# Optimization experiments

Hardware: AMD Instinct MI355X
Metric: run time of the kernel (lower is better)

## Reference

```python
import jax, jax.numpy as jnp
import numpy as np

N = 100000
E = 3200000
NFEAT, NHID, NCLASS = 512, 64, 64
K = 10
ALPHA = 0.1


def setup_inputs() -> dict:
    key = jax.random.key(0)
    ks = jax.random.split(key, 8)
    x = jax.random.normal(ks[0], (N, NFEAT), dtype=jnp.float32)
    edge_index = jax.random.randint(ks[1], (2, E), 0, N, dtype=jnp.int32)
    s1 = 1.0 / np.sqrt(NFEAT)
    W1 = jax.random.uniform(ks[2], (NFEAT, NHID), jnp.float32, -s1, s1)
    b1 = jax.random.uniform(ks[3], (NHID,), jnp.float32, -s1, s1)
    s2 = 1.0 / np.sqrt(NHID)
    W2 = jax.random.uniform(ks[4], (NHID, NCLASS), jnp.float32, -s2, s2)
    b2 = jax.random.uniform(ks[5], (NCLASS,), jnp.float32, -s2, s2)
    # PPR init of gamma coefficients: temp[k] = alpha*(1-alpha)^k, temp[K] = (1-alpha)^K
    temp = ALPHA * (1.0 - ALPHA) ** np.arange(K + 1)
    temp[-1] = (1.0 - ALPHA) ** K
    temp = jnp.asarray(temp, dtype=jnp.float32)
    return {"x": x, "edge_index": edge_index, "W1": W1, "b1": b1, "W2": W2, "b2": b2, "temp": temp}


def _gcn_norm(edge_index, num_nodes):
    # add self loops, weight 1 (PyG gcn_norm defaults)
    loop = jnp.arange(num_nodes, dtype=edge_index.dtype)
    src = jnp.concatenate([edge_index[0], loop])
    dst = jnp.concatenate([edge_index[1], loop])
    w = jnp.ones(src.shape[0], dtype=jnp.float32)
    deg = jax.ops.segment_sum(w, dst, num_segments=num_nodes)
    dinv = jnp.where(deg > 0, jax.lax.rsqrt(deg), 0.0)
    norm = dinv[src] * w * dinv[dst]
    return src, dst, norm


def reference(x, edge_index, W1, b1, W2, b2, temp):
    # MLP part (eval mode, dropout is identity)
    h = jax.nn.relu(x @ W1 + b1) @ W2 + b2  # [N, nclass]
    src, dst, norm = _gcn_norm(edge_index, x.shape[0])
    hidden = h * temp[0]
    for k in range(K):
        # gather-scale-scatter: h <- A_hat @ h
        h = jax.ops.segment_sum(norm[:, None] * h[src], dst, num_segments=x.shape[0])
        hidden = hidden + temp[k + 1] * h
    return hidden
```

## Files before the change

### kernel.cpp

```cpp
#include <hip/hip_runtime.h>

static constexpr int N = 100000;
static constexpr int E = 3200000;
static constexpr int NFEAT = 512;
static constexpr int K = 10;

typedef _Float16 half8 __attribute__((ext_vector_type(8)));
typedef _Float16 half4v __attribute__((ext_vector_type(4)));

static constexpr size_t OFF_CNT    = 0;
static constexpr size_t OFF_FILL   = 512ull * 1024;
static constexpr size_t OFF_ROWPTR = 1024ull * 1024;
static constexpr size_t OFF_DINV   = 1536ull * 1024;
static constexpr size_t OFF_BSUM   = 2048ull * 1024;
static constexpr size_t OFF_EW     = 2560ull * 1024;
static constexpr size_t OFF_GA     = OFF_EW + (size_t)E * 4 + 1024;
static constexpr size_t OFF_GB     = OFF_GA + (size_t)N * 64 * 2 + 1024;
static constexpr size_t OFF_H1     = OFF_GB + (size_t)N * 64 * 2 + 1024;

__global__ __launch_bounds__(256) void count_k(const int* __restrict__ dst,
                                               int* __restrict__ cnt) {
  int e = blockIdx.x * 256 + threadIdx.x;
  if (e < E) atomicAdd(&cnt[__builtin_nontemporal_load(dst + e)], 1);
}

__global__ __launch_bounds__(256) void dinv_k(const int* __restrict__ cnt,
                                              float* __restrict__ dinv) {
  int i = blockIdx.x * 256 + threadIdx.x;
  if (i < N) dinv[i] = 1.0f / sqrtf((float)(cnt[i] + 1));
}

__device__ inline int wave_incl_scan(int x) {
  int lane = threadIdx.x & 63;
#pragma unroll
  for (int off = 1; off < 64; off <<= 1) {
    int y = __shfl_up(x, off, 64);
    if (lane >= off) x += y;
  }
  return x;
}

__global__ __launch_bounds__(256) void scan1_k(const int* __restrict__ cnt,
                                               int* __restrict__ rowptr,
                                               int* __restrict__ bsum) {
  __shared__ int wsum[4];
  int tid = threadIdx.x, wid = tid >> 6, lane = tid & 63;
  int base = blockIdx.x * 1024 + tid * 4;
  int4 v = {0, 0, 0, 0};
  if (base + 3 < N) {
    v = *(const int4*)(cnt + base);
  } else {
    if (base + 0 < N) v.x = cnt[base + 0];
    if (base + 1 < N) v.y = cnt[base + 1];
    if (base + 2 < N) v.z = cnt[base + 2];
    if (base + 3 < N) v.w = cnt[base + 3];
  }
  int tsum = v.x + v.y + v.z + v.w;
  int incl = wave_incl_scan(tsum);
  if (lane == 63) wsum[wid] = incl;
  __syncthreads();
  int wof = 0;
  for (int i = 0; i < wid; ++i) wof += wsum[i];
  int e0 = wof + incl - tsum;
  if (base + 0 < N) rowptr[base + 0] = e0;
  if (base + 1 < N) rowptr[base + 1] = e0 + v.x;
  if (base + 2 < N) rowptr[base + 2] = e0 + v.x + v.y;
  if (base + 3 < N) rowptr[base + 3] = e0 + v.x + v.y + v.z;
  if (tid == 255) bsum[blockIdx.x] = wof + incl;
}

__global__ __launch_bounds__(128) void scan2_k(int* __restrict__ bsum) {
  __shared__ int w0sum;
  int tid = threadIdx.x, wid = tid >> 6, lane = tid & 63;
  int v = (tid < 98) ? bsum[tid] : 0;
  int incl = wave_incl_scan(v);
  if (wid == 0 && lane == 63) w0sum = incl;
  __syncthreads();
  int excl = incl - v + (wid ? w0sum : 0);
  if (tid < 98) bsum[tid] = excl;
}

__global__ __launch_bounds__(256) void scan3_k(int* __restrict__ rowptr,
                                               const int* __restrict__ bsum) {
  int i = blockIdx.x * 256 + threadIdx.x;
  if (i < N) rowptr[i] += bsum[blockIdx.x >> 2];
  if (i == 0) rowptr[N] = E;
}

__global__ __launch_bounds__(256) void fill2_k(const int* __restrict__ src,
                                               const int* __restrict__ dst,
                                               const int* __restrict__ rowptr,
                                               int* __restrict__ fillc,
                                               int* __restrict__ ew) {
  const int slice = blockIdx.x & 7;
  const int chunk = blockIdx.x >> 3;
  const int lo = slice * 12500;
  const int hi = lo + 12500;
  int e = chunk * 4096 + threadIdx.x;
  const int eend = min(E, chunk * 4096 + 4096);
  for (; e < eend; e += 256) {
    int d = __builtin_nontemporal_load(dst + e);
    if (d >= lo && d < hi) {
      int pos = rowptr[d] + atomicAdd(&fillc[d], 1);
      ew[pos] = __builtin_nontemporal_load(src + e);
    }
  }
}

__global__ __launch_bounds__(256) void gemm1_k(const float* __restrict__ x,
                                               const float* __restrict__ W1,
                                               const float* __restrict__ b1,
                                               float* __restrict__ h1) {
  __shared__ float xs[16][256];
  __shared__ float w1s[16 * 64];
  const int tid = threadIdx.x;
  const int n0 = blockIdx.x * 256;
  const int tn = tid & 127;
  const int jh = tid >> 7;
  float4 acca[8], accb[8];
#pragma unroll
  for (int i = 0; i < 8; ++i) {
    acca[i] = float4{0.f, 0.f, 0.f, 0.f};
    accb[i] = float4{0.f, 0.f, 0.f, 0.f};
  }
  const int rowA = min(n0 + tid, N - 1);
  const float* xr = x + (size_t)rowA * NFEAT;
  for (int k0 = 0; k0 < NFEAT; k0 += 16) {
    float4 a0 = *(const float4*)(xr + k0 + 0);
    float4 a1 = *(const float4*)(xr + k0 + 4);
    float4 a2 = *(const float4*)(xr + k0 + 8);
    float4 a3 = *(const float4*)(xr + k0 + 12);
    float4 wv = *(const float4*)(W1 + (size_t)k0 * 64 + tid * 4);
    __syncthreads();
    xs[0][tid] = a0.x;  xs[1][tid] = a0.y;  xs[2][tid] = a0.z;  xs[3][tid] = a0.w;
    xs[4][tid] = a1.x;  xs[5][tid] = a1.y;  xs[6][tid] = a1.z;  xs[7][tid] = a1.w;
    xs[8][tid] = a2.x;  xs[9][tid] = a2.y;  xs[10][tid] = a2.z; xs[11][tid] = a2.w;
    xs[12][tid] = a3.x; xs[13][tid] = a3.y; xs[14][tid] = a3.z; xs[15][tid] = a3.w;
    *(float4*)&w1s[tid * 4] = wv;
    __syncthreads();
#pragma unroll
    for (int kk = 0; kk < 16; ++kk) {
      float xa = xs[kk][tn];
      float xb = xs[kk][tn + 128];
      const float* wr = &w1s[kk * 64 + jh * 32];
#pragma unroll
      for (int jj = 0; jj < 8; ++jj) {
        float4 w4 = *(const float4*)(wr + jj * 4);
        acca[jj].x += xa * w4.x; acca[jj].y += xa * w4.y;
        acca[jj].z += xa * w4.z; acca[jj].w += xa * w4.w;
        accb[jj].x += xb * w4.x; accb[jj].y += xb * w4.y;
        accb[jj].z += xb * w4.z; accb[jj].w += xb * w4.w;
      }
    }
  }
  const int na = n0 + tn, nb = na + 128;
#pragma unroll
  for (int jj = 0; jj < 8; ++jj) {
    int j = jh * 32 + jj * 4;
    float4 bb = *(const float4*)(b1 + j);
    float4 ra, rb;
    ra.x = fmaxf(acca[jj].x + bb.x, 0.f); ra.y = fmaxf(acca[jj].y + bb.y, 0.f);
    ra.z = fmaxf(acca[jj].z + bb.z, 0.f); ra.w = fmaxf(acca[jj].w + bb.w, 0.f);
    rb.x = fmaxf(accb[jj].x + bb.x, 0.f); rb.y = fmaxf(accb[jj].y + bb.y, 0.f);
    rb.z = fmaxf(accb[jj].z + bb.z, 0.f); rb.w = fmaxf(accb[jj].w + bb.w, 0.f);
    if (na < N) *(float4*)(h1 + (size_t)na * 64 + j) = ra;
    if (nb < N) *(float4*)(h1 + (size_t)nb * 64 + j) = rb;
  }
}

__global__ __launch_bounds__(256) void gemm2_k(const float* __restrict__ h1,
                                               const float* __restrict__ W2,
                                               const float* __restrict__ b2,
                                               const float* __restrict__ temp,
                                               const float* __restrict__ dinv,
                                               _Float16* __restrict__ g0,
                                               float* __restrict__ out) {
  __shared__ float w2s[64 * 64];
  const int tid = threadIdx.x;
#pragma unroll
  for (int i = 0; i < 4; ++i)
    *(float4*)&w2s[(i * 256 + tid) * 4] = *(const float4*)(W2 + (size_t)(i * 256 + tid) * 4);
  __syncthreads();
  const int node = blockIdx.x * 256 + tid;
  if (node >= N) return;
  float4 acc[16];
#pragma unroll
  for (int c = 0; c < 16; ++c) acc[c] = *(const float4*)(b2 + c * 4);
  const float* hr = h1 + (size_t)node * 64;
  for (int j0 = 0; j0 < 64; j0 += 4) {
    float4 hv = *(const float4*)(hr + j0);
    float hv4[4] = {hv.x, hv.y, hv.z, hv.w};
#pragma unroll
    for (int l = 0; l < 4; ++l) {
      const float* wr = &w2s[(j0 + l) * 64];
#pragma unroll
      for (int c = 0; c < 16; ++c) {
        float4 w4 = *(const float4*)(wr + c * 4);
        acc[c].x += hv4[l] * w4.x; acc[c].y += hv4[l] * w4.y;
        acc[c].z += hv4[l] * w4.z; acc[c].w += hv4[l] * w4.w;
      }
    }
  }
  const float t0 = temp[0];
  const float di = dinv[node];
  _Float16* gp = g0 + (size_t)node * 64;
  float* op = out + (size_t)node * 64;
#pragma unroll
  for (int c = 0; c < 16; ++c) {
    float4 o;
    o.x = t0 * acc[c].x; o.y = t0 * acc[c].y;
    o.z = t0 * acc[c].z; o.w = t0 * acc[c].w;
    *(float4*)(op + c * 4) = o;
    half4v g;
    g[0] = (_Float16)(di * acc[c].x); g[1] = (_Float16)(di * acc[c].y);
    g[2] = (_Float16)(di * acc[c].z); g[3] = (_Float16)(di * acc[c].w);
    *(half4v*)(gp + c * 4) = g;
  }
}

__global__ __launch_bounds__(256) void prop_k(const _Float16* __restrict__ gin,
                                              _Float16* __restrict__ gout,
                                              float* __restrict__ out,
                                              const int* __restrict__ rowptr,
                                              const int* __restrict__ es,
                                              const float* __restrict__ dinv,
                                              const float* __restrict__ temp,
                                              int kp1, int writeh) {
  const int tid = threadIdx.x;
  const int sub = tid >> 3;
  const int l = tid & 7;
  const int node = blockIdx.x * 32 + sub;
  const int rs = rowptr[node];
  const int re = rowptr[node + 1];
  const float di = dinv[node];
  const _Float16* __restrict__ gq = gin + l * 8;

  half8 sr = *(const half8*)(gq + (size_t)node * 64);
  float a0[8], a1[8], a2[8], a3[8];
#pragma unroll
  for (int i = 0; i < 8; ++i) {
    a0[i] = (float)sr[i];
    a1[i] = 0.f; a2[i] = 0.f; a3[i] = 0.f;
  }

  int e = rs;
  for (; e + 8 <= re; e += 8) {
    int s0 = es[e],     s1 = es[e + 1], s2 = es[e + 2], s3 = es[e + 3];
    int s4 = es[e + 4], s5 = es[e + 5], s6 = es[e + 6], s7 = es[e + 7];
    half8 r0 = *(const half8*)(gq + (size_t)s0 * 64);
    half8 r1 = *(const half8*)(gq + (size_t)s1 * 64);
    half8 r2 = *(const half8*)(gq + (size_t)s2 * 64);
    half8 r3 = *(const half8*)(gq + (size_t)s3 * 64);
    half8 r4 = *(const half8*)(gq + (size_t)s4 * 64);
    half8 r5 = *(const half8*)(gq + (size_t)s5 * 64);
    half8 r6 = *(const half8*)(gq + (size_t)s6 * 64);
    half8 r7 = *(const half8*)(gq + (size_t)s7 * 64);
#pragma unroll
    for (int i = 0; i < 8; ++i) {
      a0[i] += (float)r0[i];
      a1[i] += (float)r1[i];
      a2[i] += (float)r2[i];
      a3[i] += (float)r3[i];
      a0[i] += (float)r4[i];
      a1[i] += (float)r5[i];
      a2[i] += (float)r6[i];
      a3[i] += (float)r7[i];
    }
  }
  for (; e + 4 <= re; e += 4) {
    int s0 = es[e], s1 = es[e + 1], s2 = es[e + 2], s3 = es[e + 3];
    half8 r0 = *(const half8*)(gq + (size_t)s0 * 64);
    half8 r1 = *(const half8*)(gq + (size_t)s1 * 64);
    half8 r2 = *(const half8*)(gq + (size_t)s2 * 64);
    half8 r3 = *(const half8*)(gq + (size_t)s3 * 64);
#pragma unroll
    for (int i = 0; i < 8; ++i) {
      a0[i] += (float)r0[i];
      a1[i] += (float)r1[i];
      a2[i] += (float)r2[i];
      a3[i] += (float)r3[i];
    }
  }
  for (; e < re; ++e) {
    int s0 = es[e];
    half8 r0 = *(const half8*)(gq + (size_t)s0 * 64);
#pragma unroll
    for (int i = 0; i < 8; ++i) a0[i] += (float)r0[i];
  }

  float S[8];
#pragma unroll
  for (int i = 0; i < 8; ++i) S[i] = (a0[i] + a1[i]) + (a2[i] + a3[i]);

  const float th = temp[kp1] * di;
  const float dd = di * di;
  const size_t base = (size_t)node * 64 + l * 8;
  float4 o0 = *(const float4*)(out + base);
  float4 o1 = *(const float4*)(out + base + 4);
  o0.x += th * S[0]; o0.y += th * S[1]; o0.z += th * S[2]; o0.w += th * S[3];
  o1.x += th * S[4]; o1.y += th * S[5]; o1.z += th * S[6]; o1.w += th * S[7];
  *(float4*)(out + base) = o0;
  *(float4*)(out + base + 4) = o1;
  if (writeh) {
    half8 gw;
#pragma unroll
    for (int i = 0; i < 8; ++i) gw[i] = (_Float16)(dd * S[i]);
    *(half8*)(gout + base) = gw;
  }
}

extern "C" void kernel_launch(void* const* d_in, const int* in_sizes, int n_in,
                              void* d_out, int out_size, void* d_ws, size_t ws_size,
                              hipStream_t stream) {
  const float* x = (const float*)d_in[0];
  const int* ei = (const int*)d_in[1];
  const float* W1 = (const float*)d_in[2];
  const float* b1 = (const float*)d_in[3];
  const float* W2 = (const float*)d_in[4];
  const float* b2 = (const float*)d_in[5];
  const float* temp = (const float*)d_in[6];
  const int* srcp = ei;
  const int* dstp = ei + E;

  unsigned char* ws = (unsigned char*)d_ws;
  int* cnt = (int*)(ws + OFF_CNT);
  int* fillc = (int*)(ws + OFF_FILL);
  int* rowptr = (int*)(ws + OFF_ROWPTR);
  float* dinv = (float*)(ws + OFF_DINV);
  int* bsum = (int*)(ws + OFF_BSUM);
  int* es = (int*)(ws + OFF_EW);
  _Float16* gA = (_Float16*)(ws + OFF_GA);
  _Float16* gB = (_Float16*)(ws + OFF_GB);
  float* h1 = (float*)(ws + OFF_H1);
  float* out = (float*)d_out;

  hipMemsetAsync(cnt, 0, (size_t)N * 4, stream);
  hipMemsetAsync(fillc, 0, (size_t)N * 4, stream);

  count_k<<<E / 256, 256, 0, stream>>>(dstp, cnt);
  dinv_k<<<(N + 255) / 256, 256, 0, stream>>>(cnt, dinv);
  scan1_k<<<(N + 1023) / 1024, 256, 0, stream>>>(cnt, rowptr, bsum);
  scan2_k<<<1, 128, 0, stream>>>(bsum);
  scan3_k<<<(N + 255) / 256, 256, 0, stream>>>(rowptr, bsum);
  fill2_k<<<8 * 782, 256, 0, stream>>>(srcp, dstp, rowptr, fillc, es);

  gemm1_k<<<(N + 255) / 256, 256, 0, stream>>>(x, W1, b1, h1);
  gemm2_k<<<(N + 255) / 256, 256, 0, stream>>>(h1, W2, b2, temp, dinv, gA, out);

  const _Float16* gin = gA;
  _Float16* gout = gB;
  for (int k = 0; k < K; ++k) {
    prop_k<<<N / 32, 256, 0, stream>>>(gin, gout, out, rowptr, es, dinv, temp,
                                       k + 1, (k + 1 < K) ? 1 : 0);
    _Float16* t = (_Float16*)gin;
    gin = gout;
    gout = t;
  }
}
```

Before: 1.065 ms.

## Build CSR via two-pass bucketed fill instead of sliced atomic fill

Replaces the 8-slice atomic CSR fill, which read the whole edge list eight times, with a two-pass scheme. The first pass scatters packed (src, local dst) pairs into 64-node buckets using one global atomic per bucket. The second pass sorts each bucket into exact rows using shared-memory counters. This cuts redundant edge reads and per-node global atomics, at the cost of an extra packed buffer pass and heavy contention on the bucket atomics. The packed buffer aliases h1, which gemm1 overwrites afterwards.

```diff
diff --git a/kernel.cpp b/kernel.cpp
--- a/kernel.cpp
+++ b/kernel.cpp
@@ -4,12 +4,13 @@
 static constexpr int E = 3200000;
 static constexpr int NFEAT = 512;
 static constexpr int K = 10;
+static constexpr int NB = (N + 63) / 64;
 
 typedef _Float16 half8 __attribute__((ext_vector_type(8)));
 typedef _Float16 half4v __attribute__((ext_vector_type(4)));
 
 static constexpr size_t OFF_CNT    = 0;
-static constexpr size_t OFF_FILL   = 512ull * 1024;
+static constexpr size_t OFF_BCUR   = 512ull * 1024;
 static constexpr size_t OFF_ROWPTR = 1024ull * 1024;
 static constexpr size_t OFF_DINV   = 1536ull * 1024;
 static constexpr size_t OFF_BSUM   = 2048ull * 1024;
@@ -87,23 +88,52 @@
   if (i == 0) rowptr[N] = E;
 }
 
-__global__ __launch_bounds__(256) void fill2_k(const int* __restrict__ src,
-                                               const int* __restrict__ dst,
-                                               const int* __restrict__ rowptr,
-                                               int* __restrict__ fillc,
-                                               int* __restrict__ ew) {
-  const int slice = blockIdx.x & 7;
-  const int chunk = blockIdx.x >> 3;
-  const int lo = slice * 12500;
-  const int hi = lo + 12500;
-  int e = chunk * 4096 + threadIdx.x;
-  const int eend = min(E, chunk * 4096 + 4096);
-  for (; e < eend; e += 256) {
-    int d = __builtin_nontemporal_load(dst + e);
-    if (d >= lo && d < hi) {
-      int pos = rowptr[d] + atomicAdd(&fillc[d], 1);
-      ew[pos] = __builtin_nontemporal_load(src + e);
-    }
+__global__ __launch_bounds__(256) void binit_k(const int* __restrict__ rowptr,
+                                               int* __restrict__ bcur) {
+  int b = blockIdx.x * 256 + threadIdx.x;
+  if (b < NB) bcur[b] = rowptr[b * 64];
+}
+
+__global__ __launch_bounds__(256) void fillp1_k(const int* __restrict__ src,
+                                                const int* __restrict__ dst,
+                                                int* __restrict__ bcur,
+                                                int* __restrict__ packed) {
+  int e = blockIdx.x * 256 + threadIdx.x;
+  if (e >= E) return;
+  int d = __builtin_nontemporal_load(dst + e);
+  int s = __builtin_nontemporal_load(src + e);
+  int b = d >> 6;
+  int pos = atomicAdd(&bcur[b], 1);
+  packed[pos] = (s << 6) | (d & 63);
+}
+
+__global__ __launch_bounds__(256) void fillp2_k(const int* __restrict__ rowptr,
+                                                const int* __restrict__ packed,
+                                                int* __restrict__ es) {
+  __shared__ int cl[64];
+  const int b = blockIdx.x;
+  const int n0 = b * 64;
+  const int base = rowptr[n0];
+  const int end = (n0 + 64 <= N) ? rowptr[n0 + 64] : E;
+  const int tid = threadIdx.x;
+  if (tid < 64) cl[tid] = 0;
+  __syncthreads();
+  for (int i = base + tid; i < end; i += 256)
+    atomicAdd(&cl[packed[i] & 63], 1);
+  __syncthreads();
+  if (tid == 0) {
+    int run = base;
+    for (int j = 0; j < 64; ++j) {
+      int c = cl[j];
+      cl[j] = run;
+      run += c;
+    }
+  }
+  __syncthreads();
+  for (int i = base + tid; i < end; i += 256) {
+    int p = packed[i];
+    int pos = atomicAdd(&cl[p & 63], 1);
+    es[pos] = p >> 6;
   }
 }
 
@@ -324,7 +354,7 @@
 
   unsigned char* ws = (unsigned char*)d_ws;
   int* cnt = (int*)(ws + OFF_CNT);
-  int* fillc = (int*)(ws + OFF_FILL);
+  int* bcur = (int*)(ws + OFF_BCUR);
   int* rowptr = (int*)(ws + OFF_ROWPTR);
   float* dinv = (float*)(ws + OFF_DINV);
   int* bsum = (int*)(ws + OFF_BSUM);
@@ -332,17 +362,19 @@
   _Float16* gA = (_Float16*)(ws + OFF_GA);
   _Float16* gB = (_Float16*)(ws + OFF_GB);
   float* h1 = (float*)(ws + OFF_H1);
+  int* packed = (int*)(ws + OFF_H1);
   float* out = (float*)d_out;
 
   hipMemsetAsync(cnt, 0, (size_t)N * 4, stream);
-  hipMemsetAsync(fillc, 0, (size_t)N * 4, stream);
 
   count_k<<<E / 256, 256, 0, stream>>>(dstp, cnt);
   dinv_k<<<(N + 255) / 256, 256, 0, stream>>>(cnt, dinv);
   scan1_k<<<(N + 1023) / 1024, 256, 0, stream>>>(cnt, rowptr, bsum);
   scan2_k<<<1, 128, 0, stream>>>(bsum);
   scan3_k<<<(N + 255) / 256, 256, 0, stream>>>(rowptr, bsum);
-  fill2_k<<<8 * 782, 256, 0, stream>>>(srcp, dstp, rowptr, fillc, es);
+  binit_k<<<(NB + 255) / 256, 256, 0, stream>>>(rowptr, bcur);
+  fillp1_k<<<E / 256, 256, 0, stream>>>(srcp, dstp, bcur, packed);
+  fillp2_k<<<NB, 256, 0, stream>>>(rowptr, packed, es);
 
   gemm1_k<<<(N + 255) / 256, 256, 0, stream>>>(x, W1, b1, h1);
   gemm2_k<<<(N + 255) / 256, 256, 0, stream>>>(h1, W2, b2, temp, dinv, gA, out);
```

Result: slower. 1.393 ms (+30.8%).
